# Optimization experiments

Measured on AMD Instinct MI355X. Metric: run time of the kernel, lower is better.

## Reference

```python
import jax, jax.numpy as jnp
import numpy as np

N = 50000      # nodes
E = 800000     # edges
D_IN = 128
HID = 32
HEADS = 4
D_OUT = 64
NEG_SLOPE = 0.2  # DGL GATConv default


def gat_layer(feat, W, attn_l, attn_r, bias, src, dst, H, F):
    """One DGL-style GATConv layer. feat:[N,in], W:[in,H*F], attn:[H,F], bias:[H*F]."""
    n = feat.shape[0]
    hp = (feat @ W).reshape(n, H, F)                      # projected features [N,H,F]
    el = jnp.sum(hp * attn_l, axis=-1)                    # [N,H]
    er = jnp.sum(hp * attn_r, axis=-1)                    # [N,H]
    e = jax.nn.leaky_relu(el[src] + er[dst], NEG_SLOPE)   # per-edge score [E,H]
    # segment softmax over incoming edges of each dst node
    m = jax.ops.segment_max(e, dst, num_segments=n)       # [N,H]
    a = jnp.exp(e - m[dst])
    denom = jax.ops.segment_sum(a, dst, num_segments=n)   # [N,H]
    alpha = a / denom[dst]                                # [E,H]
    msg = alpha[:, :, None] * hp[src]                     # [E,H,F]
    out = jax.ops.segment_sum(msg, dst, num_segments=n)   # [N,H,F]
    return out + bias.reshape(1, H, F)


def setup_inputs() -> dict:
    key = jax.random.key(0)
    ks = jax.random.split(key, 12)
    s = 0.05
    x = jax.random.normal(ks[0], (N, D_IN), dtype=jnp.float32)
    src = jax.random.randint(ks[1], (E,), 0, N)
    dst = jax.random.randint(ks[2], (E,), 0, N)
    # layer 1: D_IN -> HID with HEADS heads
    W1 = jax.random.normal(ks[3], (D_IN, HEADS * HID), dtype=jnp.float32) * s
    al1 = jax.random.normal(ks[4], (HEADS, HID), dtype=jnp.float32) * s
    ar1 = jax.random.normal(ks[5], (HEADS, HID), dtype=jnp.float32) * s
    b1 = jnp.zeros((HEADS * HID,), dtype=jnp.float32)
    # layer 2: HID*HEADS -> D_OUT with 1 head
    W2 = jax.random.normal(ks[6], (HID * HEADS, D_OUT), dtype=jnp.float32) * s
    al2 = jax.random.normal(ks[7], (1, D_OUT), dtype=jnp.float32) * s
    ar2 = jax.random.normal(ks[8], (1, D_OUT), dtype=jnp.float32) * s
    b2 = jnp.zeros((D_OUT,), dtype=jnp.float32)
    return {"x": x, "W1": W1, "al1": al1, "ar1": ar1, "b1": b1,
            "W2": W2, "al2": al2, "ar2": ar2, "b2": b2,
            "src": src, "dst": dst}


def reference(x, W1, al1, ar1, b1, W2, al2, ar2, b2, src, dst):
    h1 = gat_layer(x, W1, al1, ar1, b1, src, dst, HEADS, HID)   # [N,HEADS,HID]
    h1 = h1.reshape(N, HEADS * HID)                              # concat heads
    h2 = gat_layer(h1, W2, al2, ar2, b2, src, dst, 1, D_OUT)     # [N,1,D_OUT]
    return h2.reshape(N, D_OUT)                                  # squeeze head dim
```

## Files before the change

kernel.cpp:

```cpp
#include <hip/hip_runtime.h>

#define NEG_SLOPE 0.2f

typedef __attribute__((ext_vector_type(8))) short bf16x8;
typedef __attribute__((ext_vector_type(4))) float f32x4;

static __device__ __forceinline__ unsigned short f2bf(float f) {
  unsigned x = __float_as_uint(f);
  return (unsigned short)((x + 0x7FFFu + ((x >> 16) & 1u)) >> 16);
}
static __device__ __forceinline__ float bf2f(unsigned short u) {
  return __uint_as_float((unsigned)u << 16);
}

__global__ __launch_bounds__(256) void prep_kernel(const float* __restrict__ W1,
    const float* __restrict__ W2, unsigned short* __restrict__ Bp1,
    unsigned short* __restrict__ Bp2, const int* __restrict__ src,
    const int* __restrict__ dst, int* deg, int* __restrict__ rank, int E, int rankBlocks) {
  const int tid = threadIdx.x;
  if (blockIdx.x < rankBlocks) {
    const int base = blockIdx.x * 2048 + tid;
    int e[8], dv[8], r[8];
    #pragma unroll
    for (int b = 0; b < 8; ++b) e[b] = base + b * 256;
    #pragma unroll
    for (int b = 0; b < 8; ++b) if (e[b] < E) dv[b] = dst[e[b]];
    #pragma unroll
    for (int b = 0; b < 8; ++b) if (e[b] < E) r[b] = atomicAdd(&deg[dv[b]], 1);
    #pragma unroll
    for (int b = 0; b < 8; ++b) if (e[b] < E) rank[e[b]] = r[b];
    return;
  }
  const int pb = blockIdx.x - rankBlocks;
  const int lane = tid & 63, warp = tid >> 6;
  const int k0 = (lane >> 4) * 8;
  const int cl = lane & 15;
  if (pb == 0) {
    for (int f = warp; f < 32; f += 4) {
      const int ct = f >> 2, ks = f & 3;
      const int c = ct * 16 + cl;
      unsigned short t[8];
      #pragma unroll
      for (int j = 0; j < 8; ++j) t[j] = f2bf(W1[(ks * 32 + k0 + j) * 128 + c]);
      #pragma unroll
      for (int j = 0; j < 8; ++j) Bp1[((size_t)f * 64 + lane) * 8 + j] = t[j];
    }
  } else if (pb == 1) {
    for (int f = warp; f < 16; f += 4) {
      const int ct = f >> 2, ks = f & 3;
      const int c = ct * 16 + cl;
      unsigned short t[8];
      #pragma unroll
      for (int j = 0; j < 8; ++j) t[j] = f2bf(W2[(ks * 32 + k0 + j) * 64 + c]);
      #pragma unroll
      for (int j = 0; j < 8; ++j) Bp2[((size_t)f * 64 + lane) * 8 + j] = t[j];
    }
  }
}

template<int NT, bool AFP32, bool ELER>
__global__ __launch_bounds__(256) void gemm_mfma(const void* __restrict__ Asrc,
    const unsigned short* __restrict__ Bp, const float* __restrict__ al,
    const float* __restrict__ ar, unsigned short* __restrict__ hb,
    float* __restrict__ el, float* __restrict__ er, int M) {
  constexpr int CT = NT / 16;
  constexpr int LDA = 136;
  __shared__ unsigned short As[64][LDA];
  const int tid = threadIdx.x;
  const int m0 = blockIdx.x * 64;

  {
    const int r = tid >> 2, q = tid & 3;
    const int m = m0 + r;
    if constexpr (AFP32) {
      const float* A = (const float*)Asrc;
      #pragma unroll
      for (int i = 0; i < 8; ++i) {
        float4 v = make_float4(0.f, 0.f, 0.f, 0.f);
        if (m < M) v = *reinterpret_cast<const float4*>(&A[(size_t)m * 128 + q * 32 + i * 4]);
        ushort4 u;
        u.x = f2bf(v.x); u.y = f2bf(v.y); u.z = f2bf(v.z); u.w = f2bf(v.w);
        *reinterpret_cast<ushort4*>(&As[r][q * 32 + i * 4]) = u;
      }
    } else {
      const unsigned short* A = (const unsigned short*)Asrc;
      #pragma unroll
      for (int i = 0; i < 4; ++i) {
        ulonglong2 v = make_ulonglong2(0, 0);
        if (m < M) v = *reinterpret_cast<const ulonglong2*>(&A[(size_t)m * 128 + q * 32 + i * 8]);
        *reinterpret_cast<ulonglong2*>(&As[r][q * 32 + i * 8]) = v;
      }
    }
  }
  __syncthreads();

  const int w = tid >> 6, lane = tid & 63;
  const int arow = w * 16 + (lane & 15);
  const int koff = (lane >> 4) * 8;
  f32x4 acc[CT];
  #pragma unroll
  for (int ct = 0; ct < CT; ++ct) acc[ct] = (f32x4){0.f, 0.f, 0.f, 0.f};

  #pragma unroll
  for (int ks = 0; ks < 4; ++ks) {
    const bf16x8 af = *reinterpret_cast<const bf16x8*>(&As[arow][ks * 32 + koff]);
    #pragma unroll
    for (int ct = 0; ct < CT; ++ct) {
      const bf16x8 bfr = *reinterpret_cast<const bf16x8*>(&Bp[((size_t)(ct * 4 + ks) * 64 + lane) * 8]);
      acc[ct] = __builtin_amdgcn_mfma_f32_16x16x32_bf16(af, bfr, acc[ct], 0, 0, 0);
    }
  }

  const int rbase = m0 + w * 16 + (lane >> 4) * 4;
  const int cl = lane & 15;
  #pragma unroll
  for (int ct = 0; ct < CT; ++ct) {
    const int c = ct * 16 + cl;
    #pragma unroll
    for (int reg = 0; reg < 4; ++reg) {
      const int m = rbase + reg;
      if (m < M) hb[(size_t)m * NT + c] = f2bf(acc[ct][reg]);
    }
  }
  if constexpr (ELER) {
    float alv[CT], arv[CT];
    #pragma unroll
    for (int ct = 0; ct < CT; ++ct) { alv[ct] = al[ct * 16 + cl]; arv[ct] = ar[ct * 16 + cl]; }
    #pragma unroll
    for (int reg = 0; reg < 4; ++reg) {
      float pl = 0.f, pr = 0.f;
      #pragma unroll
      for (int ct = 0; ct < CT; ++ct) {
        pl = fmaf(alv[ct], acc[ct][reg], pl);
        pr = fmaf(arv[ct], acc[ct][reg], pr);
      }
      #pragma unroll
      for (int off = 1; off < 16; off <<= 1) {
        pl += __shfl_xor(pl, off);
        pr += __shfl_xor(pr, off);
      }
      const int m = rbase + reg;
      if (cl == 0 && m < M) { el[m] = pl; er[m] = pr; }
    }
  }
}

__global__ __launch_bounds__(256) void block_sum_kernel(const int* __restrict__ deg,
    int* __restrict__ partials, int N) {
  __shared__ int wsum[4];
  const int tid = threadIdx.x;
  const int base = blockIdx.x * 1024 + tid * 4;
  int s = 0;
  #pragma unroll
  for (int j = 0; j < 4; ++j) if (base + j < N) s += deg[base + j];
  #pragma unroll
  for (int off = 32; off >= 1; off >>= 1) s += __shfl_down(s, off);
  if ((tid & 63) == 0) wsum[tid >> 6] = s;
  __syncthreads();
  if (tid == 0) partials[blockIdx.x] = wsum[0] + wsum[1] + wsum[2] + wsum[3];
}

__global__ __launch_bounds__(64) void scan_partials_kernel(int* partials, int nb) {
  const int tid = threadIdx.x;
  int v = (tid < nb) ? partials[tid] : 0;
  int incl = v;
  #pragma unroll
  for (int off = 1; off < 64; off <<= 1) {
    const int t = __shfl_up(incl, off);
    if (tid >= off) incl += t;
  }
  if (tid < nb) partials[tid] = incl - v;
}

__global__ __launch_bounds__(256) void block_scan_kernel(const int* __restrict__ deg,
    const int* __restrict__ partials, int* __restrict__ row_ptr, int N, int E) {
  __shared__ int wtot[4];
  const int tid = threadIdx.x;
  const int lane = tid & 63, wid = tid >> 6;
  const int idx = blockIdx.x * 1024 + tid * 4;
  int v[4];
  #pragma unroll
  for (int j = 0; j < 4; ++j) v[j] = (idx + j < N) ? deg[idx + j] : 0;
  const int tsum = v[0] + v[1] + v[2] + v[3];
  int incl = tsum;
  #pragma unroll
  for (int off = 1; off < 64; off <<= 1) {
    const int t = __shfl_up(incl, off);
    if (lane >= off) incl += t;
  }
  if (lane == 63) wtot[wid] = incl;
  __syncthreads();
  int excl = partials[blockIdx.x] + incl - tsum;
  for (int w = 0; w < wid; ++w) excl += wtot[w];
  #pragma unroll
  for (int j = 0; j < 4; ++j) {
    if (idx + j < N) { row_ptr[idx + j] = excl; excl += v[j]; }
  }
  if (blockIdx.x == 0 && tid == 0) row_ptr[N] = E;
}

__global__ __launch_bounds__(256) void place_eler_kernel(const int* __restrict__ src,
    const int* __restrict__ dst, const int* __restrict__ row_ptr,
    const int* __restrict__ rank, unsigned short* __restrict__ csr_src, int E,
    int placeBlocks, const unsigned short* __restrict__ hb1,
    const float* __restrict__ al1, const float* __restrict__ ar1,
    float* __restrict__ el1, float* __restrict__ er1, int N) {
  const int tid = threadIdx.x;
  if (blockIdx.x < placeBlocks) {
    const int e = blockIdx.x * 256 + tid;
    if (e < E) csr_src[row_ptr[dst[e]] + rank[e]] = (unsigned short)src[e];
    return;
  }
  const int idx = (blockIdx.x - placeBlocks) * 256 + tid;
  if (idx >= N * 4) return;
  const int h = idx & 3;
  const unsigned short* row = hb1 + (size_t)(idx >> 2) * 128 + h * 32;
  float sl = 0.f, sr = 0.f;
  #pragma unroll
  for (int f = 0; f < 32; ++f) {
    const float v = bf2f(row[f]);
    sl = fmaf(al1[h * 32 + f], v, sl);
    sr = fmaf(ar1[h * 32 + f], v, sr);
  }
  el1[idx] = sl; er1[idx] = sr;
}

template<int H, int F, int NPW, bool OBF>
__global__ __launch_bounds__(256) void gat_agg(const int* __restrict__ row_ptr,
    const unsigned short* __restrict__ csr_src, const float* __restrict__ el,
    const float* __restrict__ er, const unsigned short* __restrict__ hb,
    const float* __restrict__ bias, void* __restrict__ outp, int N) {
  constexpr int HF = H * F;
  constexpr int LPN = 64 / NPW;
  constexpr int CPL = HF / LPN;
  static_assert(CPL == 4, "CPL must be 4");
  const int wid = threadIdx.x >> 6;
  const int lane = threadIdx.x & 63;
  const int g = lane / LPN;
  const int gl = lane % LPN;
  const int d = (blockIdx.x * 4 + wid) * NPW + g;
  if (d >= N) return;
  const int c0 = gl * CPL;
  const int h = c0 / F;
  const float erd = er[(size_t)d * H + h];
  const int beg = row_ptr[d], end = row_ptr[d + 1];
  float a0 = 0.f, a1 = 0.f, a2 = 0.f, a3 = 0.f, denom = 0.f;
  int i = beg;

  for (; i + 16 <= end; i += 16) {
    int s[16];
    #pragma unroll
    for (int j = 0; j < 16; ++j) s[j] = csr_src[i + j];
    float ee[16];
    #pragma unroll
    for (int j = 0; j < 16; ++j) ee[j] = el[(size_t)s[j] * H + h];
    ushort4 u[16];
    #pragma unroll
    for (int j = 0; j < 16; ++j)
      u[j] = *reinterpret_cast<const ushort4*>(&hb[(size_t)s[j] * HF + c0]);
    #pragma unroll
    for (int j = 0; j < 16; ++j) {
      float t = ee[j] + erd;
      t = fmaxf(t, NEG_SLOPE * t);
      const float x = __expf(t);
      denom += x;
      a0 = fmaf(x, bf2f(u[j].x), a0); a1 = fmaf(x, bf2f(u[j].y), a1);
      a2 = fmaf(x, bf2f(u[j].z), a2); a3 = fmaf(x, bf2f(u[j].w), a3);
    }
  }
  for (; i + 8 <= end; i += 8) {
    int s[8];
    #pragma unroll
    for (int j = 0; j < 8; ++j) s[j] = csr_src[i + j];
    float ee[8];
    #pragma unroll
    for (int j = 0; j < 8; ++j) ee[j] = el[(size_t)s[j] * H + h];
    ushort4 u[8];
    #pragma unroll
    for (int j = 0; j < 8; ++j)
      u[j] = *reinterpret_cast<const ushort4*>(&hb[(size_t)s[j] * HF + c0]);
    #pragma unroll
    for (int j = 0; j < 8; ++j) {
      float t = ee[j] + erd;
      t = fmaxf(t, NEG_SLOPE * t);
      const float x = __expf(t);
      denom += x;
      a0 = fmaf(x, bf2f(u[j].x), a0); a1 = fmaf(x, bf2f(u[j].y), a1);
      a2 = fmaf(x, bf2f(u[j].z), a2); a3 = fmaf(x, bf2f(u[j].w), a3);
    }
  }
  for (; i + 4 <= end; i += 4) {
    int s[4];
    #pragma unroll
    for (int j = 0; j < 4; ++j) s[j] = csr_src[i + j];
    float ee[4];
    #pragma unroll
    for (int j = 0; j < 4; ++j) ee[j] = el[(size_t)s[j] * H + h];
    ushort4 u[4];
    #pragma unroll
    for (int j = 0; j < 4; ++j)
      u[j] = *reinterpret_cast<const ushort4*>(&hb[(size_t)s[j] * HF + c0]);
    #pragma unroll
    for (int j = 0; j < 4; ++j) {
      float t = ee[j] + erd;
      t = fmaxf(t, NEG_SLOPE * t);
      const float x = __expf(t);
      denom += x;
      a0 = fmaf(x, bf2f(u[j].x), a0); a1 = fmaf(x, bf2f(u[j].y), a1);
      a2 = fmaf(x, bf2f(u[j].z), a2); a3 = fmaf(x, bf2f(u[j].w), a3);
    }
  }
  for (; i < end; ++i) {
    const int s = csr_src[i];
    float t = el[(size_t)s * H + h] + erd;
    t = fmaxf(t, NEG_SLOPE * t);
    const float x = __expf(t);
    denom += x;
    const ushort4 u = *reinterpret_cast<const ushort4*>(&hb[(size_t)s * HF + c0]);
    a0 = fmaf(x, bf2f(u.x), a0); a1 = fmaf(x, bf2f(u.y), a1);
    a2 = fmaf(x, bf2f(u.z), a2); a3 = fmaf(x, bf2f(u.w), a3);
  }

  const float inv = denom > 0.f ? 1.f / denom : 0.f;
  const float4 bv = *reinterpret_cast<const float4*>(&bias[c0]);
  if constexpr (OBF) {
    ushort4 o;
    o.x = f2bf(bv.x + a0 * inv); o.y = f2bf(bv.y + a1 * inv);
    o.z = f2bf(bv.z + a2 * inv); o.w = f2bf(bv.w + a3 * inv);
    *reinterpret_cast<ushort4*>(&((unsigned short*)outp)[(size_t)d * HF + c0]) = o;
  } else {
    float4 o;
    o.x = bv.x + a0 * inv; o.y = bv.y + a1 * inv;
    o.z = bv.z + a2 * inv; o.w = bv.w + a3 * inv;
    *reinterpret_cast<float4*>(&((float*)outp)[(size_t)d * HF + c0]) = o;
  }
}

extern "C" void kernel_launch(void* const* d_in, const int* in_sizes, int n_in,
                              void* d_out, int out_size, void* d_ws, size_t ws_size,
                              hipStream_t stream) {
  const float* x   = (const float*)d_in[0];
  const float* W1  = (const float*)d_in[1];
  const float* al1 = (const float*)d_in[2];
  const float* ar1 = (const float*)d_in[3];
  const float* b1  = (const float*)d_in[4];
  const float* W2  = (const float*)d_in[5];
  const float* al2 = (const float*)d_in[6];
  const float* ar2 = (const float*)d_in[7];
  const float* b2  = (const float*)d_in[8];
  const int* src   = (const int*)d_in[9];
  const int* dst   = (const int*)d_in[10];
  const int N = in_sizes[0] / 128;
  const int E = in_sizes[9];
  float* out = (float*)d_out;

  char* wp = (char*)d_ws;
  auto alloc = [&wp](size_t bytes) {
    char* r = wp;
    wp += (bytes + 31) & ~size_t(31);
    return r;
  };
  float* el1  = (float*)alloc((size_t)N * 4 * sizeof(float));
  float* er1  = (float*)alloc((size_t)N * 4 * sizeof(float));
  float* el2  = (float*)alloc((size_t)N * sizeof(float));
  float* er2  = (float*)alloc((size_t)N * sizeof(float));
  int* deg     = (int*)alloc((size_t)N * sizeof(int));
  int* row_ptr = (int*)alloc((size_t)(N + 1) * sizeof(int));
  int* rank    = (int*)alloc((size_t)E * sizeof(int));
  int* partials = (int*)alloc(64 * sizeof(int));
  unsigned short* csr_src = (unsigned short*)alloc((size_t)E * sizeof(unsigned short));
  unsigned short* out1b   = (unsigned short*)alloc((size_t)N * 128 * sizeof(unsigned short));
  unsigned short* hb1     = (unsigned short*)alloc((size_t)N * 128 * sizeof(unsigned short));
  unsigned short* hb2     = (unsigned short*)alloc((size_t)N * 64 * sizeof(unsigned short));
  unsigned short* Bp1     = (unsigned short*)alloc(128 * 128 * sizeof(unsigned short));
  unsigned short* Bp2     = (unsigned short*)alloc(128 * 64 * sizeof(unsigned short));

  const dim3 blk(256);
  const int nb = (N + 1023) / 1024;
  const int gemmBlocks = (N + 63) / 64;
  const int rankBlocks = (E + 2047) / 2048;
  const int placeBlocks = (E + 255) / 256;
  const int elerBlocks = (N * 4 + 255) / 256;

  hipMemsetAsync(deg, 0, (size_t)N * sizeof(int), stream);
  prep_kernel<<<dim3(rankBlocks + 2), blk, 0, stream>>>(W1, W2, Bp1, Bp2, src, dst, deg, rank, E, rankBlocks);

  gemm_mfma<128, true, false><<<dim3(gemmBlocks), blk, 0, stream>>>(
      x, Bp1, nullptr, nullptr, hb1, nullptr, nullptr, N);

  block_sum_kernel<<<dim3(nb), blk, 0, stream>>>(deg, partials, N);
  scan_partials_kernel<<<dim3(1), dim3(64), 0, stream>>>(partials, nb);
  block_scan_kernel<<<dim3(nb), blk, 0, stream>>>(deg, partials, row_ptr, N, E);
  place_eler_kernel<<<dim3(placeBlocks + elerBlocks), blk, 0, stream>>>(
      src, dst, row_ptr, rank, csr_src, E, placeBlocks, hb1, al1, ar1, el1, er1, N);

  gat_agg<4, 32, 2, true><<<dim3((N + 7) / 8), blk, 0, stream>>>(
      row_ptr, csr_src, el1, er1, hb1, b1, out1b, N);

  gemm_mfma<64, false, true><<<dim3(gemmBlocks), blk, 0, stream>>>(
      out1b, Bp2, al2, ar2, hb2, el2, er2, N);
  gat_agg<1, 64, 4, false><<<dim3((N + 15) / 16), blk, 0, stream>>>(
      row_ptr, csr_src, el2, er2, hb2, b2, out, N);
}
```

Measured before the change: 164.8 us.

## Fuse layer-1 el/er into GEMM, merge rank pass into GEMM launch, fold scans

The layer-1 el/er computation moves out of the placement kernel and into the GEMM epilogue, computed per head from the fp32 accumulators instead of re-reading bf16 hb1. The edge-rank atomic pass now runs as extra blocks of the layer-1 GEMM launch, and the deg memset becomes blocks of the weight-prep kernel. The partial scan is folded into block_scan so each block rescans the partials itself. Together these remove the memset, one launch and a round trip through hb1. The cost is heterogeneous blocks inside one grid and el1/er1 now computed from unrounded values.

```diff
diff --git a/kernel.cpp b/kernel.cpp
--- a/kernel.cpp
+++ b/kernel.cpp
@@ -13,29 +13,19 @@
   return __uint_as_float((unsigned)u << 16);
 }
 
-__global__ __launch_bounds__(256) void prep_kernel(const float* __restrict__ W1,
+__global__ __launch_bounds__(256) void prep0_kernel(const float* __restrict__ W1,
     const float* __restrict__ W2, unsigned short* __restrict__ Bp1,
-    unsigned short* __restrict__ Bp2, const int* __restrict__ src,
-    const int* __restrict__ dst, int* deg, int* __restrict__ rank, int E, int rankBlocks) {
+    unsigned short* __restrict__ Bp2, int4* __restrict__ deg4, int n4) {
   const int tid = threadIdx.x;
-  if (blockIdx.x < rankBlocks) {
-    const int base = blockIdx.x * 2048 + tid;
-    int e[8], dv[8], r[8];
-    #pragma unroll
-    for (int b = 0; b < 8; ++b) e[b] = base + b * 256;
-    #pragma unroll
-    for (int b = 0; b < 8; ++b) if (e[b] < E) dv[b] = dst[e[b]];
-    #pragma unroll
-    for (int b = 0; b < 8; ++b) if (e[b] < E) r[b] = atomicAdd(&deg[dv[b]], 1);
-    #pragma unroll
-    for (int b = 0; b < 8; ++b) if (e[b] < E) rank[e[b]] = r[b];
+  const int lane = tid & 63, warp = tid >> 6;
+  if (blockIdx.x >= 2) {
+    const int i = (blockIdx.x - 2) * 256 + tid;
+    if (i < n4) deg4[i] = make_int4(0, 0, 0, 0);
     return;
   }
-  const int pb = blockIdx.x - rankBlocks;
-  const int lane = tid & 63, warp = tid >> 6;
   const int k0 = (lane >> 4) * 8;
   const int cl = lane & 15;
-  if (pb == 0) {
+  if (blockIdx.x == 0) {
     for (int f = warp; f < 32; f += 4) {
       const int ct = f >> 2, ks = f & 3;
       const int c = ct * 16 + cl;
@@ -45,7 +35,7 @@
       #pragma unroll
       for (int j = 0; j < 8; ++j) Bp1[((size_t)f * 64 + lane) * 8 + j] = t[j];
     }
-  } else if (pb == 1) {
+  } else {
     for (int f = warp; f < 16; f += 4) {
       const int ct = f >> 2, ks = f & 3;
       const int c = ct * 16 + cl;
@@ -58,16 +48,35 @@
   }
 }
 
-template<int NT, bool AFP32, bool ELER>
+template<int NT, int H, bool AFP32, bool RANK>
 __global__ __launch_bounds__(256) void gemm_mfma(const void* __restrict__ Asrc,
     const unsigned short* __restrict__ Bp, const float* __restrict__ al,
     const float* __restrict__ ar, unsigned short* __restrict__ hb,
-    float* __restrict__ el, float* __restrict__ er, int M) {
+    float* __restrict__ el, float* __restrict__ er, int M,
+    int rankBlocks, const int* __restrict__ dst, int* deg, int* __restrict__ rank, int E) {
   constexpr int CT = NT / 16;
+  constexpr int CPH = CT / H;
   constexpr int LDA = 136;
   __shared__ unsigned short As[64][LDA];
   const int tid = threadIdx.x;
-  const int m0 = blockIdx.x * 64;
+
+  if constexpr (RANK) {
+    if (blockIdx.x < rankBlocks) {
+      const int base = blockIdx.x * 2048 + tid;
+      int e[8], dv[8], r[8];
+      #pragma unroll
+      for (int b = 0; b < 8; ++b) e[b] = base + b * 256;
+      #pragma unroll
+      for (int b = 0; b < 8; ++b) if (e[b] < E) dv[b] = dst[e[b]];
+      #pragma unroll
+      for (int b = 0; b < 8; ++b) if (e[b] < E) r[b] = atomicAdd(&deg[dv[b]], 1);
+      #pragma unroll
+      for (int b = 0; b < 8; ++b) if (e[b] < E) rank[e[b]] = r[b];
+      return;
+    }
+  }
+  const int bx = RANK ? (blockIdx.x - rankBlocks) : blockIdx.x;
+  const int m0 = bx * 64;
 
   {
     const int r = tid >> 2, q = tid & 3;
@@ -122,15 +131,18 @@
       if (m < M) hb[(size_t)m * NT + c] = f2bf(acc[ct][reg]);
     }
   }
-  if constexpr (ELER) {
-    float alv[CT], arv[CT];
-    #pragma unroll
-    for (int ct = 0; ct < CT; ++ct) { alv[ct] = al[ct * 16 + cl]; arv[ct] = ar[ct * 16 + cl]; }
-    #pragma unroll
-    for (int reg = 0; reg < 4; ++reg) {
+  float alv[CT], arv[CT];
+  #pragma unroll
+  for (int ct = 0; ct < CT; ++ct) { alv[ct] = al[ct * 16 + cl]; arv[ct] = ar[ct * 16 + cl]; }
+  #pragma unroll
+  for (int reg = 0; reg < 4; ++reg) {
+    const int m = rbase + reg;
+    #pragma unroll
+    for (int h = 0; h < H; ++h) {
       float pl = 0.f, pr = 0.f;
       #pragma unroll
-      for (int ct = 0; ct < CT; ++ct) {
+      for (int t = 0; t < CPH; ++t) {
+        const int ct = h * CPH + t;
         pl = fmaf(alv[ct], acc[ct][reg], pl);
         pr = fmaf(arv[ct], acc[ct][reg], pr);
       }
@@ -139,8 +151,7 @@
         pl += __shfl_xor(pl, off);
         pr += __shfl_xor(pr, off);
       }
-      const int m = rbase + reg;
-      if (cl == 0 && m < M) { el[m] = pl; er[m] = pr; }
+      if (cl == 0 && m < M) { el[(size_t)m * H + h] = pl; er[(size_t)m * H + h] = pr; }
     }
   }
 }
@@ -160,23 +171,22 @@
   if (tid == 0) partials[blockIdx.x] = wsum[0] + wsum[1] + wsum[2] + wsum[3];
 }
 
-__global__ __launch_bounds__(64) void scan_partials_kernel(int* partials, int nb) {
-  const int tid = threadIdx.x;
-  int v = (tid < nb) ? partials[tid] : 0;
-  int incl = v;
-  #pragma unroll
-  for (int off = 1; off < 64; off <<= 1) {
-    const int t = __shfl_up(incl, off);
-    if (tid >= off) incl += t;
-  }
-  if (tid < nb) partials[tid] = incl - v;
-}
-
 __global__ __launch_bounds__(256) void block_scan_kernel(const int* __restrict__ deg,
-    const int* __restrict__ partials, int* __restrict__ row_ptr, int N, int E) {
+    const int* __restrict__ partials, int* __restrict__ row_ptr, int N, int E, int nb) {
   __shared__ int wtot[4];
+  __shared__ int myoff;
   const int tid = threadIdx.x;
   const int lane = tid & 63, wid = tid >> 6;
+  if (tid < 64) {
+    int v = (tid < nb) ? partials[tid] : 0;
+    int incl = v;
+    #pragma unroll
+    for (int off = 1; off < 64; off <<= 1) {
+      const int t = __shfl_up(incl, off);
+      if (tid >= off) incl += t;
+    }
+    if (tid == blockIdx.x) myoff = incl - v;
+  }
   const int idx = blockIdx.x * 1024 + tid * 4;
   int v[4];
   #pragma unroll
@@ -190,7 +200,7 @@
   }
   if (lane == 63) wtot[wid] = incl;
   __syncthreads();
-  int excl = partials[blockIdx.x] + incl - tsum;
+  int excl = myoff + incl - tsum;
   for (int w = 0; w < wid; ++w) excl += wtot[w];
   #pragma unroll
   for (int j = 0; j < 4; ++j) {
@@ -199,30 +209,11 @@
   if (blockIdx.x == 0 && tid == 0) row_ptr[N] = E;
 }
 
-__global__ __launch_bounds__(256) void place_eler_kernel(const int* __restrict__ src,
+__global__ __launch_bounds__(256) void place_kernel(const int* __restrict__ src,
     const int* __restrict__ dst, const int* __restrict__ row_ptr,
-    const int* __restrict__ rank, unsigned short* __restrict__ csr_src, int E,
-    int placeBlocks, const unsigned short* __restrict__ hb1,
-    const float* __restrict__ al1, const float* __restrict__ ar1,
-    float* __restrict__ el1, float* __restrict__ er1, int N) {
-  const int tid = threadIdx.x;
-  if (blockIdx.x < placeBlocks) {
-    const int e = blockIdx.x * 256 + tid;
-    if (e < E) csr_src[row_ptr[dst[e]] + rank[e]] = (unsigned short)src[e];
-    return;
-  }
-  const int idx = (blockIdx.x - placeBlocks) * 256 + tid;
-  if (idx >= N * 4) return;
-  const int h = idx & 3;
-  const unsigned short* row = hb1 + (size_t)(idx >> 2) * 128 + h * 32;
-  float sl = 0.f, sr = 0.f;
-  #pragma unroll
-  for (int f = 0; f < 32; ++f) {
-    const float v = bf2f(row[f]);
-    sl = fmaf(al1[h * 32 + f], v, sl);
-    sr = fmaf(ar1[h * 32 + f], v, sr);
-  }
-  el1[idx] = sl; er1[idx] = sr;
+    const int* __restrict__ rank, unsigned short* __restrict__ csr_src, int E) {
+  const int e = blockIdx.x * 256 + threadIdx.x;
+  if (e < E) csr_src[row_ptr[dst[e]] + rank[e]] = (unsigned short)src[e];
 }
 
 template<int H, int F, int NPW, bool OBF>
@@ -364,7 +355,7 @@
   float* er1  = (float*)alloc((size_t)N * 4 * sizeof(float));
   float* el2  = (float*)alloc((size_t)N * sizeof(float));
   float* er2  = (float*)alloc((size_t)N * sizeof(float));
-  int* deg     = (int*)alloc((size_t)N * sizeof(int));
+  int* deg     = (int*)alloc((size_t)((N + 3) & ~3) * sizeof(int));
   int* row_ptr = (int*)alloc((size_t)(N + 1) * sizeof(int));
   int* rank    = (int*)alloc((size_t)E * sizeof(int));
   int* partials = (int*)alloc(64 * sizeof(int));
@@ -380,25 +371,25 @@
   const int gemmBlocks = (N + 63) / 64;
   const int rankBlocks = (E + 2047) / 2048;
   const int placeBlocks = (E + 255) / 256;
-  const int elerBlocks = (N * 4 + 255) / 256;
-
-  hipMemsetAsync(deg, 0, (size_t)N * sizeof(int), stream);
-  prep_kernel<<<dim3(rankBlocks + 2), blk, 0, stream>>>(W1, W2, Bp1, Bp2, src, dst, deg, rank, E, rankBlocks);
-
-  gemm_mfma<128, true, false><<<dim3(gemmBlocks), blk, 0, stream>>>(
-      x, Bp1, nullptr, nullptr, hb1, nullptr, nullptr, N);
+  const int n4 = (N + 3) / 4;
+  const int zeroBlocks = (n4 + 255) / 256;
+
+  prep0_kernel<<<dim3(2 + zeroBlocks), blk, 0, stream>>>(W1, W2, Bp1, Bp2, (int4*)deg, n4);
+
+  gemm_mfma<128, 4, true, true><<<dim3(rankBlocks + gemmBlocks), blk, 0, stream>>>(
+      x, Bp1, al1, ar1, hb1, el1, er1, N, rankBlocks, dst, deg, rank, E);
 
   block_sum_kernel<<<dim3(nb), blk, 0, stream>>>(deg, partials, N);
-  scan_partials_kernel<<<dim3(1), dim3(64), 0, stream>>>(partials, nb);
-  block_scan_kernel<<<dim3(nb), blk, 0, stream>>>(deg, partials, row_ptr, N, E);
-  place_eler_kernel<<<dim3(placeBlocks + elerBlocks), blk, 0, stream>>>(
-      src, dst, row_ptr, rank, csr_src, E, placeBlocks, hb1, al1, ar1, el1, er1, N);
+  block_scan_kernel<<<dim3(nb), blk, 0, stream>>>(deg, partials, row_ptr, N, E, nb);
+
+  place_kernel<<<dim3(placeBlocks), blk, 0, stream>>>(src, dst, row_ptr, rank, csr_src, E);
 
   gat_agg<4, 32, 2, true><<<dim3((N + 7) / 8), blk, 0, stream>>>(
       row_ptr, csr_src, el1, er1, hb1, b1, out1b, N);
 
-  gemm_mfma<64, false, true><<<dim3(gemmBlocks), blk, 0, stream>>>(
-      out1b, Bp2, al2, ar2, hb2, el2, er2, N);
+  gemm_mfma<64, 1, false, false><<<dim3(gemmBlocks), blk, 0, stream>>>(
+      out1b, Bp2, al2, ar2, hb2, el2, er2, N, 0, nullptr, nullptr, nullptr, 0);
+
   gat_agg<1, 64, 4, false><<<dim3((N + 15) / 16), blk, 0, stream>>>(
       row_ptr, csr_src, el2, er2, hb2, b2, out, N);
 }
```

After: 152.3 us. -7.6%, faster.
